# Optimization experiments

Measured on AMD Instinct MI355X. Metric: run time of the kernel, lower is better.

Reference implementation:

```python
import jax, jax.numpy as jnp
import numpy as np


def setup_inputs() -> dict:
    key = jax.random.key(0)
    k1, k2 = jax.random.split(key)
    B, T, H, D = 2, 2048, 16, 64          # batch, seq, heads, head_dim
    NUM_HASHES, NUM_BUCKETS = 4, 64
    hidden_states = jax.random.normal(k1, (B, T, H * D), dtype=jnp.float32)
    # equivalent of torch.randn rotations with fixed hash_seed
    random_rotations = jax.random.normal(k2, (H, D, NUM_HASHES, NUM_BUCKETS // 2), dtype=jnp.float32)
    return {"hidden_states": hidden_states, "random_rotations": random_rotations}


def reference(hidden_states, random_rotations):
    # hidden_states: [B, T, H*D]; random_rotations: [H, D, num_hashes, num_buckets//2]
    H, D, num_hashes, half = random_rotations.shape
    B, T, _ = hidden_states.shape
    # _split_hidden_size_dim: [B,T,H*D] -> [B,H,T,D]
    v = hidden_states.reshape(B, T, H, D).transpose(0, 2, 1, 3)
    # rotated: [B, H, num_hashes, T, num_buckets//2]
    rotated = jnp.einsum('bhtd,hdnr->bhntr', v, random_rotations)
    rotated = jnp.concatenate([rotated, -rotated], axis=-1)  # [..., num_buckets]
    buckets = jnp.argmax(rotated, axis=-1)                   # [B, H, num_hashes, T]
    b = buckets.transpose(0, 1, 3, 2)                        # [B, H, T, num_hashes]
    # m[b,h,i,j] = any_n (bucket_n(i) == bucket_n(j)); OR-accumulate over the
    # small fixed num_hashes axis to avoid a [B,H,T,T,num_hashes] intermediate.
    m = jnp.zeros((B, H, T, T), dtype=bool)
    for n in range(num_hashes):
        bn = b[..., n]
        m = m | (bn[:, :, :, None] == bn[:, :, None, :])
    return m
```

## Files before the change

kernel.cpp:

```cpp
#include <hip/hip_runtime.h>
#include <stdint.h>

#define BB 2
#define HH 16
#define TT 2048
#define DD 64
#define NHASH 4
#define NHALF 32

__global__ __launch_bounds__(256, 2) void lsh_buckets_kernel(
    const float* __restrict__ hs,
    const float* __restrict__ rot,
    uint32_t* __restrict__ words)
{
    __shared__ double rot_d[NHASH * NHALF * DD];

    const int blk  = blockIdx.x;
    const int bh   = blk >> 5;
    const int tblk = blk & 31;
    const int b    = bh >> 4;
    const int h    = bh & 15;
    const int t0   = tblk * 64;
    const int tid  = threadIdx.x;
    const int n    = tid >> 6;
    const int lt   = tid & 63;

    {
        const float* rh = rot + (size_t)h * (DD * NHASH * NHALF);
        for (int k = tid; k < NHASH * NHALF * DD; k += 256) {
            const int d  = k & 63;
            const int nr = k >> 6;
            rot_d[k] = (double)rh[d * (NHASH * NHALF) + nr];
        }
    }

    const int t = t0 + lt;
    const float* vp = hs + ((size_t)(b * TT + t)) * (HH * DD) + h * DD;
    double vd[DD];
    #pragma unroll
    for (int d4 = 0; d4 < 16; ++d4) {
        const float4 f = ((const float4*)vp)[d4];
        vd[d4 * 4 + 0] = (double)f.x;
        vd[d4 * 4 + 1] = (double)f.y;
        vd[d4 * 4 + 2] = (double)f.z;
        vd[d4 * 4 + 3] = (double)f.w;
    }
    __syncthreads();

    const double* cb = rot_d + n * (NHALF * DD);
    float fmx = -INFINITY; int imx = 0;
    float fmn =  INFINITY; int imn = 0;
    for (int r = 0; r < NHALF; ++r) {
        const double* c = cb + r * DD;
        double a0 = 0.0, a1 = 0.0, a2 = 0.0, a3 = 0.0;
        #pragma unroll
        for (int d = 0; d < DD; d += 4) {
            a0 += vd[d + 0] * c[d + 0];
            a1 += vd[d + 1] * c[d + 1];
            a2 += vd[d + 2] * c[d + 2];
            a3 += vd[d + 3] * c[d + 3];
        }
        const float f = (float)((a0 + a1) + (a2 + a3));
        if (f > fmx) { fmx = f; imx = r; }
        if (f < fmn) { fmn = f; imn = r; }
    }
    const uint32_t bucket = (fmx >= -fmn) ? (uint32_t)imx : (uint32_t)(NHALF + imn);

    __syncthreads();
    uint32_t* bk = (uint32_t*)rot_d;
    bk[n * 64 + lt] = bucket;
    __syncthreads();
    if (tid < 64) {
        words[(size_t)bh * TT + t0 + tid] = bk[0 * 64 + tid]
                                          | (bk[1 * 64 + tid] << 8)
                                          | (bk[2 * 64 + tid] << 16)
                                          | (bk[3 * 64 + tid] << 24);
    }
}

#define ROWS 8
__device__ __forceinline__ uint32_t eq_any_byte(uint32_t a, uint32_t b) {
    const uint32_t x = a ^ b;
    return ((x - 0x01010101u) & ~x & 0x80808080u) ? 1u : 0u;
}

__global__ __launch_bounds__(256) void lsh_mask_kernel(
    const uint32_t* __restrict__ words,
    uint4* __restrict__ out)
{
    const int bh  = blockIdx.x >> 8;
    const int i0  = (blockIdx.x & 255) * ROWS;
    const int tid = threadIdx.x;
    const uint32_t* wrow = words + (bh << 11);

    const uint4 wj0 = ((const uint4*)wrow)[tid];
    const uint4 wj1 = ((const uint4*)wrow)[tid + 256];

    #pragma unroll
    for (int k = 0; k < ROWS; ++k) {
        const uint32_t wi = wrow[i0 + k];
        uint4 r0, r1;
        r0.x = eq_any_byte(wi, wj0.x); r0.y = eq_any_byte(wi, wj0.y);
        r0.z = eq_any_byte(wi, wj0.z); r0.w = eq_any_byte(wi, wj0.w);
        r1.x = eq_any_byte(wi, wj1.x); r1.y = eq_any_byte(wi, wj1.y);
        r1.z = eq_any_byte(wi, wj1.z); r1.w = eq_any_byte(wi, wj1.w);
        uint4* op = out + (((size_t)((bh << 11) + i0 + k)) << 9);
        op[tid]       = r0;
        op[tid + 256] = r1;
    }
}

extern "C" void kernel_launch(void* const* d_in, const int* in_sizes, int n_in,
                              void* d_out, int out_size, void* d_ws, size_t ws_size,
                              hipStream_t stream) {
    const float* hs  = (const float*)d_in[0];
    const float* rot = (const float*)d_in[1];
    uint32_t* words  = (uint32_t*)d_ws;

    lsh_buckets_kernel<<<BB * HH * (TT / 64), 256, 0, stream>>>(hs, rot, words);
    lsh_mask_kernel<<<BB * HH * (TT / ROWS), 256, 0, stream>>>(words, (uint4*)d_out);
}
```

Baseline: 153.7 us.

## Register-tile the bucket projection with swizzled float LDS staging

The bucket kernel now stages both the hidden-state tile and the rotations in LDS as fp32 with XOR swizzles, instead of as a double rotation table. Each thread computes an 8x4 tile of double-precision dot products, converting to double in registers. The per-thread argmax/argmin results are then reduced across the 8 rotation groups through LDS. The goal is to cut LDS footprint and per-element LDS reads through register reuse, which should raise occupancy. In exchange it adds a second reduction stage, extra barriers and more register pressure from the 32 double accumulators.

```diff
diff --git a/kernel.cpp b/kernel.cpp
--- a/kernel.cpp
+++ b/kernel.cpp
@@ -13,7 +13,9 @@
     const float* __restrict__ rot,
     uint32_t* __restrict__ words)
 {
-    __shared__ double rot_d[NHASH * NHALF * DD];
+    __shared__ uint32_t lds[12288];
+    float4* v4 = (float4*)lds;
+    float4* r4 = (float4*)(lds + 4096);
 
     const int blk  = blockIdx.x;
     const int bh   = blk >> 5;
@@ -23,58 +25,112 @@
     const int t0   = tblk * 64;
     const int tid  = threadIdx.x;
     const int n    = tid >> 6;
-    const int lt   = tid & 63;
+    const int lane = tid & 63;
+    const int tg   = lane >> 3;
+    const int rg   = lane & 7;
 
+    #pragma unroll
+    for (int p = 0; p < 4; ++p) {
+        const int k  = tid + p * 256;
+        const int t  = k >> 4;
+        const int d4 = k & 15;
+        const float4 f = ((const float4*)(hs + ((size_t)(b * TT + t0 + t)) * (HH * DD) + h * DD))[d4];
+        v4[t * 16 + (d4 ^ (t >> 3))] = f;
+    }
     {
         const float* rh = rot + (size_t)h * (DD * NHASH * NHALF);
-        for (int k = tid; k < NHASH * NHALF * DD; k += 256) {
-            const int d  = k & 63;
-            const int nr = k >> 6;
-            rot_d[k] = (double)rh[d * (NHASH * NHALF) + nr];
+        float* rf = (float*)r4;
+        #pragma unroll
+        for (int p = 0; p < 32; ++p) {
+            const int g  = tid + p * 256;
+            const int d  = g >> 7;
+            const int nr = g & 127;
+            const int nn = nr >> 5;
+            const int r  = nr & 31;
+            const int slot = (d >> 2) ^ (r >> 2);
+            rf[((nn * 32 + r) * 16 + slot) * 4 + (d & 3)] = rh[g];
+        }
+    }
+    __syncthreads();
+
+    double acc[8][4];
+    #pragma unroll
+    for (int i = 0; i < 8; ++i)
+        #pragma unroll
+        for (int j = 0; j < 4; ++j) acc[i][j] = 0.0;
+
+    const int vbase = tg * 8 * 16;
+    const int rbase = (n * 32 + rg * 4) * 16;
+
+    for (int s = 0; s < 16; ++s) {
+        double rd[4][4];
+        #pragma unroll
+        for (int j = 0; j < 4; ++j) {
+            const float4 rf = r4[rbase + j * 16 + (s ^ rg)];
+            rd[j][0] = (double)rf.x; rd[j][1] = (double)rf.y;
+            rd[j][2] = (double)rf.z; rd[j][3] = (double)rf.w;
+        }
+        #pragma unroll
+        for (int i = 0; i < 8; ++i) {
+            const float4 vf = v4[vbase + i * 16 + (s ^ tg)];
+            const double v0 = (double)vf.x, v1 = (double)vf.y;
+            const double v2 = (double)vf.z, v3 = (double)vf.w;
+            #pragma unroll
+            for (int j = 0; j < 4; ++j) {
+                acc[i][j] += v0 * rd[j][0];
+                acc[i][j] += v1 * rd[j][1];
+                acc[i][j] += v2 * rd[j][2];
+                acc[i][j] += v3 * rd[j][3];
+            }
         }
     }
 
-    const int t = t0 + lt;
-    const float* vp = hs + ((size_t)(b * TT + t)) * (HH * DD) + h * DD;
-    double vd[DD];
+    __syncthreads();
+    float*    vmaxL = (float*)lds;
+    float*    vminL = (float*)(lds + 2304);
+    uint32_t* imaxL = lds + 4608;
+    uint32_t* iminL = lds + 6912;
+    uint32_t* bkt   = lds + 9216;
+
     #pragma unroll
-    for (int d4 = 0; d4 < 16; ++d4) {
-        const float4 f = ((const float4*)vp)[d4];
-        vd[d4 * 4 + 0] = (double)f.x;
-        vd[d4 * 4 + 1] = (double)f.y;
-        vd[d4 * 4 + 2] = (double)f.z;
-        vd[d4 * 4 + 3] = (double)f.w;
+    for (int i = 0; i < 8; ++i) {
+        const int t = tg * 8 + i;
+        float fmx = -INFINITY; int imx = 0;
+        float fmn =  INFINITY; int imn = 0;
+        #pragma unroll
+        for (int j = 0; j < 4; ++j) {
+            const float f = (float)acc[i][j];
+            const int   r = rg * 4 + j;
+            if (f > fmx) { fmx = f; imx = r; }
+            if (f < fmn) { fmn = f; imn = r; }
+        }
+        const int o = (n * 64 + t) * 9 + rg;
+        vmaxL[o] = fmx; vminL[o] = fmn;
+        imaxL[o] = (uint32_t)imx; iminL[o] = (uint32_t)imn;
     }
     __syncthreads();
-
-    const double* cb = rot_d + n * (NHALF * DD);
-    float fmx = -INFINITY; int imx = 0;
-    float fmn =  INFINITY; int imn = 0;
-    for (int r = 0; r < NHALF; ++r) {
-        const double* c = cb + r * DD;
-        double a0 = 0.0, a1 = 0.0, a2 = 0.0, a3 = 0.0;
+    {
+        const int nn = tid >> 6;
+        const int t  = tid & 63;
+        float fmx = -INFINITY; int imx = 0;
+        float fmn =  INFINITY; int imn = 0;
         #pragma unroll
-        for (int d = 0; d < DD; d += 4) {
-            a0 += vd[d + 0] * c[d + 0];
-            a1 += vd[d + 1] * c[d + 1];
-            a2 += vd[d + 2] * c[d + 2];
-            a3 += vd[d + 3] * c[d + 3];
+        for (int g = 0; g < 8; ++g) {
+            const int o = (nn * 64 + t) * 9 + g;
+            const float fx = vmaxL[o];
+            const float fn = vminL[o];
+            if (fx > fmx) { fmx = fx; imx = (int)imaxL[o]; }
+            if (fn < fmn) { fmn = fn; imn = (int)iminL[o]; }
         }
-        const float f = (float)((a0 + a1) + (a2 + a3));
-        if (f > fmx) { fmx = f; imx = r; }
-        if (f < fmn) { fmn = f; imn = r; }
+        const uint32_t bucket = (fmx >= -fmn) ? (uint32_t)imx : (uint32_t)(NHALF + imn);
+        bkt[nn * 64 + t] = bucket;
     }
-    const uint32_t bucket = (fmx >= -fmn) ? (uint32_t)imx : (uint32_t)(NHALF + imn);
-
-    __syncthreads();
-    uint32_t* bk = (uint32_t*)rot_d;
-    bk[n * 64 + lt] = bucket;
     __syncthreads();
     if (tid < 64) {
-        words[(size_t)bh * TT + t0 + tid] = bk[0 * 64 + tid]
-                                          | (bk[1 * 64 + tid] << 8)
-                                          | (bk[2 * 64 + tid] << 16)
-                                          | (bk[3 * 64 + tid] << 24);
+        words[(size_t)bh * TT + t0 + tid] = bkt[tid]
+                                          | (bkt[64  + tid] << 8)
+                                          | (bkt[128 + tid] << 16)
+                                          | (bkt[192 + tid] << 24);
     }
 }
 
```

Measured after the change: 133.8 us. -13.0%, faster.
